# Kernel optimization log

Hardware: AMD Instinct MI355X
Metric: run time of the kernel (lower is better)

The kernel has to match this reference:

```python
import jax, jax.numpy as jnp
import numpy as np

N = 512
B = 128
T = 1000
INP = 6
OUT = 1
DT, TAU = 1.0, 10.0
ALPHA = DT / TAU
SIGMA_REC, SIGMA_INP = 0.05, 0.01
SPECTRAL_RAD = 1.2


def setup_inputs() -> dict:
    key = jax.random.key(0)
    k_u, k_rn, k_in, k_wr, k_wi, k_wo = jax.random.split(key, 6)
    u = jax.random.normal(k_u, (B, T, INP), dtype=jnp.float32)
    # noise pre-scaled as in the torch module: sqrt(2/alpha * sigma^2) * randn
    rec_noise = jnp.sqrt(2.0 / ALPHA * SIGMA_REC ** 2) * jax.random.normal(k_rn, (B, T, N), dtype=jnp.float32)
    inp_noise = jnp.sqrt(2.0 / ALPHA * SIGMA_INP ** 2) * jax.random.normal(k_in, (B, T, INP), dtype=jnp.float32)
    # scaled init connectivity (stand-in for get_connectivity): spectral radius ~ SPECTRAL_RAD
    W_rec = (SPECTRAL_RAD / np.sqrt(N)) * jax.random.normal(k_wr, (N, N), dtype=jnp.float32)
    W_inp = (1.0 / np.sqrt(INP)) * jax.random.normal(k_wi, (N, INP), dtype=jnp.float32)
    W_out = (1.0 / np.sqrt(N)) * jax.random.normal(k_wo, (OUT, N), dtype=jnp.float32)
    y_init = jnp.zeros((N,), dtype=jnp.float32)
    return {"u": u, "rec_noise": rec_noise, "inp_noise": inp_noise,
            "W_rec": W_rec, "W_inp": W_inp, "W_out": W_out, "y_init": y_init}


def _run_dynamics(u, rec_noise, inp_noise, W_rec, W_inp, W_out, y_init):
    alpha = jnp.float32(ALPHA)
    s0 = jnp.broadcast_to(y_init, (u.shape[0], N))  # (B, N)

    def step(s, xs):
        u_t, in_t, rn_t = xs  # (B,INP),(B,INP),(B,N)
        pre = s @ W_rec.T + (u_t + in_t) @ W_inp.T
        s_new = (1.0 - alpha) * s + alpha * (jax.nn.relu(pre) + rn_t)
        return s_new, s_new

    # torch loop runs for i in range(T-1); step i uses inputs/noise at time i
    xs = (jnp.swapaxes(u[:, :-1], 0, 1),
          jnp.swapaxes(inp_noise[:, :-1], 0, 1),
          jnp.swapaxes(rec_noise[:, :-1], 0, 1))
    _, states_tail = jax.lax.scan(step, s0, xs)  # (T-1, B, N)
    states = jnp.concatenate([s0[:, None, :], jnp.swapaxes(states_tail, 0, 1)], axis=1)  # (B, T, N)
    outputs = states @ W_out.T  # (B, T, OUT)
    return states, outputs


def reference(u, rec_noise, inp_noise, W_rec, W_inp, W_out, y_init):
    return _run_dynamics(u, rec_noise, inp_noise, W_rec, W_inp, W_out, y_init)
```

## Files before the change

kernel.cpp:

```cpp
#include <hip/hip_runtime.h>


#define NN 512
#define BB 128
#define TT 1000
#define NIN 6
#define PP 4
#define GG 2
#define NGRP (BB / GG)
#define NWG (PP * NGRP)
#define SLICE (NN / PP)
#define XWORDS (2 * NGRP * GG * NN)
#define WS_NEED (XWORDS * sizeof(unsigned long long))

typedef unsigned long long u64;

__global__ void init_xbuf(u64* xbuf) {
  const int i = blockIdx.x * 256 + threadIdx.x;
  if (i < XWORDS / 2) {
    xbuf[i] = 0xFFFFFFFF00000000ULL;
    xbuf[i + XWORDS / 2] = 0xFFFFFFFF00000000ULL;
  }
}

__device__ __forceinline__ float wave_sum(float v) {
  #pragma unroll
  for (int off = 32; off > 0; off >>= 1) v += __shfl_xor(v, off, 64);
  return v;
}

__device__ __forceinline__ void pin4(float4& a, float4& b, float4& c, float4& d) {
  asm volatile("" : "+v"(a.x), "+v"(a.y), "+v"(a.z), "+v"(a.w),
                    "+v"(b.x), "+v"(b.y), "+v"(b.z), "+v"(b.w),
                    "+v"(c.x), "+v"(c.y), "+v"(c.z), "+v"(c.w),
                    "+v"(d.x), "+v"(d.y), "+v"(d.z), "+v"(d.w));
}

__device__ __forceinline__ u64 xld(const u64* p) {
  return __hip_atomic_load(p, __ATOMIC_RELAXED, __HIP_MEMORY_SCOPE_SYSTEM);
}
__device__ __forceinline__ void xst(u64* p, u64 v) {
  __hip_atomic_store(p, v, __ATOMIC_RELAXED, __HIP_MEMORY_SCOPE_SYSTEM);
}

__global__ __launch_bounds__(512, 1)
void rnn_tagx2(const float* __restrict__ u, const float* __restrict__ rnz,
               const float* __restrict__ inz, const float* __restrict__ Wrec,
               const float* __restrict__ Winp, const float* __restrict__ yinit,
               float* __restrict__ states, u64* __restrict__ xbuf) {
  const int tid = threadIdx.x;
  const int xcd = blockIdx.x & 7;
  const int rest = blockIdx.x >> 3;
  const int p = rest & 3;
  const int g = (rest >> 2) * 8 + xcd;

  const int nq = tid & 31;
  const int n0 = nq << 2;
  const int ks = tid >> 5;
  const int k0 = ks << 5;
  const int ub = (tid >> 7) & 1;
  const int un = tid & 127;
  const int ung = p * SLICE + un;
  const int f1r = tid >> 8, f1b = (tid >> 7) & 1, f1n = tid & 127;
  const int f1q = (p + 1 + f1r) & 3;
  const int f2b = (tid >> 7) & 1, f2n = tid & 127;
  const int f2q = (p + 3) & 3;

  __shared__ __align__(16) float pred[16][GG][SLICE];
  __shared__ __align__(16) float s_all[GG][NN];
  __shared__ float winp_s[SLICE][NIN];
  __shared__ float ubuf[2][GG][NIN];

  float4 w[4][8];
  #pragma unroll
  for (int i = 0; i < 4; ++i) {
    const float* wr = Wrec + (size_t)(p * SLICE + n0 + i) * NN + k0;
    #pragma unroll
    for (int q = 0; q < 8; ++q)
      w[i][q] = *reinterpret_cast<const float4*>(wr + 4 * q);
  }
  for (int i = tid; i < SLICE * NIN; i += 512) {
    const int r = i / NIN, j = i - r * NIN;
    winp_s[r][j] = Winp[(p * SLICE + r) * NIN + j];
  }
  for (int i = tid; i < GG * NN; i += 512)
    s_all[i >> 9][i & 511] = yinit[i & 511];
  for (int i = tid; i < GG * NN; i += 512)
    states[(size_t)(g * GG + (i >> 9)) * TT * NN + (i & 511)] = yinit[i & 511];
  float scur = (tid < 256) ? yinit[ung] : 0.f;
  __syncthreads();

  for (int t = 0; t < TT - 1; ++t) {
    const int par = t & 1;

    #pragma unroll
    for (int i = 0; i < 4; ++i) {
      pin4(w[i][0], w[i][1], w[i][2], w[i][3]);
      pin4(w[i][4], w[i][5], w[i][6], w[i][7]);
    }

    float rnv = 0.f;
    if (tid < 256)
      rnv = rnz[((size_t)(g * GG + ub) * TT + t) * NN + ung];
    if (tid < GG * NIN) {
      const int b = tid / NIN, j = tid - b * NIN;
      const size_t idx = ((size_t)(g * GG + b) * TT + t) * NIN + j;
      ubuf[par][b][j] = u[idx] + inz[idx];
    }

    if (t > 0) {
      const u64* xb = xbuf + ((size_t)par * NGRP + g) * GG * NN;
      const u64* p1 = xb + (size_t)f1b * NN + f1q * SLICE + f1n;
      u64 v1 = xld(p1);
      u64 v2 = 0;
      const u64* p2 = xb + (size_t)f2b * NN + f2q * SLICE + f2n;
      if (tid < 256) v2 = xld(p2);
      while ((int)(v1 >> 32) < t) { __builtin_amdgcn_s_sleep(1); v1 = xld(p1); }
      s_all[f1b][f1q * SLICE + f1n] = __uint_as_float((unsigned)v1);
      if (tid < 256) {
        while ((int)(v2 >> 32) < t) { __builtin_amdgcn_s_sleep(1); v2 = xld(p2); }
        s_all[f2b][f2q * SLICE + f2n] = __uint_as_float((unsigned)v2);
      }
    }
    __syncthreads();

    float a0[GG], a1[GG], a2[GG], a3[GG];
    #pragma unroll
    for (int b = 0; b < GG; ++b) { a0[b] = 0.f; a1[b] = 0.f; a2[b] = 0.f; a3[b] = 0.f; }
    #pragma unroll
    for (int b = 0; b < GG; ++b) {
      #pragma unroll
      for (int q = 0; q < 8; ++q) {
        const float4 sv = *reinterpret_cast<const float4*>(&s_all[b][k0 + 4 * q]);
        a0[b] = fmaf(w[0][q].x, sv.x, a0[b]); a0[b] = fmaf(w[0][q].y, sv.y, a0[b]);
        a0[b] = fmaf(w[0][q].z, sv.z, a0[b]); a0[b] = fmaf(w[0][q].w, sv.w, a0[b]);
        a1[b] = fmaf(w[1][q].x, sv.x, a1[b]); a1[b] = fmaf(w[1][q].y, sv.y, a1[b]);
        a1[b] = fmaf(w[1][q].z, sv.z, a1[b]); a1[b] = fmaf(w[1][q].w, sv.w, a1[b]);
        a2[b] = fmaf(w[2][q].x, sv.x, a2[b]); a2[b] = fmaf(w[2][q].y, sv.y, a2[b]);
        a2[b] = fmaf(w[2][q].z, sv.z, a2[b]); a2[b] = fmaf(w[2][q].w, sv.w, a2[b]);
        a3[b] = fmaf(w[3][q].x, sv.x, a3[b]); a3[b] = fmaf(w[3][q].y, sv.y, a3[b]);
        a3[b] = fmaf(w[3][q].z, sv.z, a3[b]); a3[b] = fmaf(w[3][q].w, sv.w, a3[b]);
      }
    }
    #pragma unroll
    for (int b = 0; b < GG; ++b)
      *reinterpret_cast<float4*>(&pred[ks][b][n0]) =
          make_float4(a0[b], a1[b], a2[b], a3[b]);
    __syncthreads();

    if (tid < 256) {
      float pre = 0.f;
      #pragma unroll
      for (int q = 0; q < 16; ++q) pre += pred[q][ub][un];
      #pragma unroll
      for (int j = 0; j < NIN; ++j)
        pre = fmaf(ubuf[par][ub][j], winp_s[un][j], pre);
      const float sn = 0.9f * scur + 0.1f * (fmaxf(pre, 0.f) + rnv);
      states[((size_t)(g * GG + ub) * TT + t + 1) * NN + ung] = sn;
      const u64 pw = ((u64)(unsigned)(t + 1) << 32) | __float_as_uint(sn);
      xst(&xbuf[(((size_t)((t + 1) & 1) * NGRP + g) * GG + ub) * NN + ung], pw);
      asm volatile("" ::: "memory");
      s_all[ub][ung] = sn;
      scur = sn;
    }
  }
}

__global__ __launch_bounds__(256)
void out_proj(const float* __restrict__ states, const float* __restrict__ Wout,
              float* __restrict__ outputs) {
  const int lane = threadIdx.x & 63;
  const size_t row = (size_t)blockIdx.x * 4 + (threadIdx.x >> 6);
  if (row >= (size_t)BB * TT) return;
  const float* sr = states + row * NN;
  float acc = 0.f;
  #pragma unroll
  for (int h = 0; h < 2; ++h) {
    const float4 sv = *reinterpret_cast<const float4*>(sr + h * 256 + lane * 4);
    const float4 wv = *reinterpret_cast<const float4*>(Wout + h * 256 + lane * 4);
    acc = fmaf(sv.x, wv.x, acc);
    acc = fmaf(sv.y, wv.y, acc);
    acc = fmaf(sv.z, wv.z, acc);
    acc = fmaf(sv.w, wv.w, acc);
  }
  acc = wave_sum(acc);
  if (lane == 0) outputs[row] = acc;
}

__global__ __launch_bounds__(512)
void rnn_fused(const float* __restrict__ u, const float* __restrict__ rnz,
               const float* __restrict__ inz, const float* __restrict__ Wsrc,
               const float* __restrict__ Winp, const float* __restrict__ Wout,
               const float* __restrict__ yinit,
               float* __restrict__ states, float* __restrict__ outputs) {
  const int tid = threadIdx.x;
  const int n4 = tid & 127;
  const int kc = tid >> 7;
  const int b0 = blockIdx.x * 2;
  const int b1 = b0 + 1;

  __shared__ __align__(16) float s[2][NN];
  __shared__ __align__(16) float red[2][128][20];
  __shared__ float ubf[2 * NIN];
  __shared__ float outred[2][8];

  float wi[NIN];
  #pragma unroll
  for (int j = 0; j < NIN; ++j) wi[j] = Winp[tid * NIN + j];
  const float wo = Wout[tid];
  const float yv = yinit[tid];

  s[0][tid] = yv;
  s[1][tid] = yv;
  states[(size_t)(b0 * TT) * NN + tid] = yv;
  states[(size_t)(b1 * TT) * NN + tid] = yv;
  {
    float pzz = wave_sum(yv * wo);
    if ((tid & 63) == 0) outred[0][tid >> 6] = pzz;
  }
  __syncthreads();
  if (tid < 2) {
    float a = 0.f;
    #pragma unroll
    for (int wq = 0; wq < 8; ++wq) a += outred[0][wq];
    outputs[(tid ? b1 : b0) * TT] = a;
  }
  __syncthreads();

  for (int t = 0; t < TT - 1; ++t) {
    const float rn0 = rnz[(size_t)(b0 * TT + t) * NN + tid];
    const float rn1 = rnz[(size_t)(b1 * TT + t) * NN + tid];
    float uv = 0.f;
    if (tid < 2 * NIN) {
      const int b = (tid < NIN) ? b0 : b1;
      const int j = (tid < NIN) ? tid : tid - NIN;
      const int idx = (b * TT + t) * NIN + j;
      uv = u[idx] + inz[idx];
    }
    float a0[4] = {0.f, 0.f, 0.f, 0.f};
    float a1[4] = {0.f, 0.f, 0.f, 0.f};
    const int kbase0 = kc * 128;
    #pragma unroll 4
    for (int j4 = 0; j4 < 32; ++j4) {
      const int kb = kbase0 + j4 * 4;
      const float4 s0v = *reinterpret_cast<const float4*>(&s[0][kb]);
      const float4 s1v = *reinterpret_cast<const float4*>(&s[1][kb]);
      const float s0a[4] = {s0v.x, s0v.y, s0v.z, s0v.w};
      const float s1a[4] = {s1v.x, s1v.y, s1v.z, s1v.w};
      #pragma unroll
      for (int jj = 0; jj < 4; ++jj) {
        const int k = kb + jj;
        const float* pw = Wsrc + (size_t)(n4 << 2) * NN + k;
        float4 wv;
        wv.x = pw[0]; wv.y = pw[NN]; wv.z = pw[2 * NN]; wv.w = pw[3 * NN];
        a0[0] = fmaf(wv.x, s0a[jj], a0[0]);
        a0[1] = fmaf(wv.y, s0a[jj], a0[1]);
        a0[2] = fmaf(wv.z, s0a[jj], a0[2]);
        a0[3] = fmaf(wv.w, s0a[jj], a0[3]);
        a1[0] = fmaf(wv.x, s1a[jj], a1[0]);
        a1[1] = fmaf(wv.y, s1a[jj], a1[1]);
        a1[2] = fmaf(wv.z, s1a[jj], a1[2]);
        a1[3] = fmaf(wv.w, s1a[jj], a1[3]);
      }
    }
    if (tid < 2 * NIN) ubf[tid] = uv;
    *reinterpret_cast<float4*>(&red[0][n4][kc << 2]) =
        make_float4(a0[0], a0[1], a0[2], a0[3]);
    *reinterpret_cast<float4*>(&red[1][n4][kc << 2]) =
        make_float4(a1[0], a1[1], a1[2], a1[3]);
    __syncthreads();
    const int n = tid;
    const int r = n >> 2, c = n & 3;
    float pre0 = (red[0][r][c] + red[0][r][4 + c]) +
                 (red[0][r][8 + c] + red[0][r][12 + c]);
    float pre1 = (red[1][r][c] + red[1][r][4 + c]) +
                 (red[1][r][8 + c] + red[1][r][12 + c]);
    #pragma unroll
    for (int j = 0; j < NIN; ++j) {
      pre0 = fmaf(ubf[j], wi[j], pre0);
      pre1 = fmaf(ubf[NIN + j], wi[j], pre1);
    }
    const float sn0 = 0.9f * s[0][n] + 0.1f * (fmaxf(pre0, 0.f) + rn0);
    const float sn1 = 0.9f * s[1][n] + 0.1f * (fmaxf(pre1, 0.f) + rn1);
    states[(size_t)(b0 * TT + t + 1) * NN + n] = sn0;
    states[(size_t)(b1 * TT + t + 1) * NN + n] = sn1;
    s[0][n] = sn0;
    s[1][n] = sn1;
    float p0 = wave_sum(sn0 * wo);
    float p1 = wave_sum(sn1 * wo);
    if ((tid & 63) == 0) {
      outred[0][tid >> 6] = p0;
      outred[1][tid >> 6] = p1;
    }
    __syncthreads();
    if (tid < 2) {
      float a = 0.f;
      #pragma unroll
      for (int wq = 0; wq < 8; ++wq) a += outred[tid][wq];
      outputs[(tid ? b1 : b0) * TT + t + 1] = a;
    }
  }
}

extern "C" void kernel_launch(void* const* d_in, const int* in_sizes, int n_in,
                              void* d_out, int out_size, void* d_ws, size_t ws_size,
                              hipStream_t stream) {
  const float* u    = (const float*)d_in[0];
  const float* rnz  = (const float*)d_in[1];
  const float* inz  = (const float*)d_in[2];
  const float* Wrec = (const float*)d_in[3];
  const float* Winp = (const float*)d_in[4];
  const float* Wout = (const float*)d_in[5];
  const float* yin  = (const float*)d_in[6];
  float* states  = (float*)d_out;
  float* outputs = states + (size_t)BB * TT * NN;

  if (ws_size >= WS_NEED) {
    u64* xbuf = (u64*)d_ws;
    init_xbuf<<<(XWORDS / 2 + 255) / 256, 256, 0, stream>>>(xbuf);
    rnn_tagx2<<<NWG, 512, 0, stream>>>(u, rnz, inz, Wrec, Winp, yin,
                                       states, xbuf);
    out_proj<<<(BB * TT + 3) / 4, 256, 0, stream>>>(states, Wout, outputs);
  } else {
    rnn_fused<<<BB / 2, 512, 0, stream>>>(u, rnz, inz, Wrec, Winp, Wout,
                                          yin, states, outputs);
  }
}
```

Baseline: 2.862 ms.

## Add fast sc0-scoped exchange buffer with fallback to system-scope polling

Adds a second exchange buffer written and read with inline-asm global loads and stores using the sc0 cache bit instead of system-scope atomics, for cross-workgroup state handoff each timestep. Readers poll the fast buffer a few times and permanently fall back to the system-scope buffer if the tag has not arrived. The aim is to cut the latency of inter-workgroup synchronisation on the serial recurrence. In exchange every state value is written twice, the workspace requirement doubles, and the fast path depends on cache coherence behaviour that may not hold across XCDs.

```diff
diff --git a/kernel.cpp b/kernel.cpp
--- a/kernel.cpp
+++ b/kernel.cpp
@@ -11,16 +11,14 @@
 #define NWG (PP * NGRP)
 #define SLICE (NN / PP)
 #define XWORDS (2 * NGRP * GG * NN)
-#define WS_NEED (XWORDS * sizeof(unsigned long long))
+#define WS_FAST (2 * XWORDS * sizeof(unsigned long long))
+#define WS_SLOW (XWORDS * sizeof(unsigned long long))
 
 typedef unsigned long long u64;
 
-__global__ void init_xbuf(u64* xbuf) {
+__global__ void init_xbuf(u64* xbuf, int nwords) {
   const int i = blockIdx.x * 256 + threadIdx.x;
-  if (i < XWORDS / 2) {
-    xbuf[i] = 0xFFFFFFFF00000000ULL;
-    xbuf[i + XWORDS / 2] = 0xFFFFFFFF00000000ULL;
-  }
+  if (i < nwords) xbuf[i] = 0xFFFFFFFF00000000ULL;
 }
 
 __device__ __forceinline__ float wave_sum(float v) {
@@ -42,12 +40,45 @@
 __device__ __forceinline__ void xst(u64* p, u64 v) {
   __hip_atomic_store(p, v, __ATOMIC_RELAXED, __HIP_MEMORY_SCOPE_SYSTEM);
 }
-
+__device__ __forceinline__ u64 fld(const u64* p) {
+  u64 v;
+  asm volatile("global_load_dwordx2 %0, %1, off sc0\n\ts_waitcnt vmcnt(0)"
+               : "=v"(v) : "v"(p) : "memory");
+  return v;
+}
+__device__ __forceinline__ void fst(u64* p, u64 v) {
+  asm volatile("global_store_dwordx2 %0, %1, off sc0" :: "v"(p), "v"(v)
+               : "memory");
+}
+
+__device__ __forceinline__ u64 pollw(const u64* pf, const u64* ps, int t,
+                                     int& fastok) {
+  u64 v;
+  if (fastok) {
+    v = fld(pf);
+    #pragma unroll 1
+    for (int tr = 0; tr < 4 && (int)(v >> 32) < t; ++tr) {
+      __builtin_amdgcn_s_sleep(1);
+      v = fld(pf);
+    }
+    if ((int)(v >> 32) >= t) return v;
+    fastok = 0;
+  }
+  v = xld(ps);
+  while ((int)(v >> 32) < t) {
+    __builtin_amdgcn_s_sleep(2);
+    v = xld(ps);
+  }
+  return v;
+}
+
+template <bool TWOSIDED>
 __global__ __launch_bounds__(512, 1)
-void rnn_tagx2(const float* __restrict__ u, const float* __restrict__ rnz,
+void rnn_tagx3(const float* __restrict__ u, const float* __restrict__ rnz,
                const float* __restrict__ inz, const float* __restrict__ Wrec,
                const float* __restrict__ Winp, const float* __restrict__ yinit,
-               float* __restrict__ states, u64* __restrict__ xbuf) {
+               float* __restrict__ states, u64* __restrict__ xslow,
+               u64* __restrict__ xfast) {
   const int tid = threadIdx.x;
   const int xcd = blockIdx.x & 7;
   const int rest = blockIdx.x >> 3;
@@ -88,6 +119,7 @@
   for (int i = tid; i < GG * NN; i += 512)
     states[(size_t)(g * GG + (i >> 9)) * TT * NN + (i & 511)] = yinit[i & 511];
   float scur = (tid < 256) ? yinit[ung] : 0.f;
+  int fastok = TWOSIDED ? 1 : 0;
   __syncthreads();
 
   for (int t = 0; t < TT - 1; ++t) {
@@ -109,16 +141,13 @@
     }
 
     if (t > 0) {
-      const u64* xb = xbuf + ((size_t)par * NGRP + g) * GG * NN;
-      const u64* p1 = xb + (size_t)f1b * NN + f1q * SLICE + f1n;
-      u64 v1 = xld(p1);
-      u64 v2 = 0;
-      const u64* p2 = xb + (size_t)f2b * NN + f2q * SLICE + f2n;
-      if (tid < 256) v2 = xld(p2);
-      while ((int)(v1 >> 32) < t) { __builtin_amdgcn_s_sleep(1); v1 = xld(p1); }
+      const size_t base = ((size_t)par * NGRP + g) * GG * NN;
+      const size_t o1 = base + (size_t)f1b * NN + f1q * SLICE + f1n;
+      const u64 v1 = pollw(xfast + o1, xslow + o1, t, fastok);
       s_all[f1b][f1q * SLICE + f1n] = __uint_as_float((unsigned)v1);
       if (tid < 256) {
-        while ((int)(v2 >> 32) < t) { __builtin_amdgcn_s_sleep(1); v2 = xld(p2); }
+        const size_t o2 = base + (size_t)f2b * NN + f2q * SLICE + f2n;
+        const u64 v2 = pollw(xfast + o2, xslow + o2, t, fastok);
         s_all[f2b][f2q * SLICE + f2n] = __uint_as_float((unsigned)v2);
       }
     }
@@ -139,7 +168,7 @@
         a2[b] = fmaf(w[2][q].x, sv.x, a2[b]); a2[b] = fmaf(w[2][q].y, sv.y, a2[b]);
         a2[b] = fmaf(w[2][q].z, sv.z, a2[b]); a2[b] = fmaf(w[2][q].w, sv.w, a2[b]);
         a3[b] = fmaf(w[3][q].x, sv.x, a3[b]); a3[b] = fmaf(w[3][q].y, sv.y, a3[b]);
-        a3[b] = fmaf(w[3][q].z, sv.z, a3[b]); a3[b] = fmaf(w[3][q].w, sv.w, a3[b]);
+        a3[b] = fmaf(w[3][q].w, sv.w, a3[b]); a3[b] = fmaf(w[3][q].z, sv.z, a3[b]);
       }
     }
     #pragma unroll
@@ -158,7 +187,9 @@
       const float sn = 0.9f * scur + 0.1f * (fmaxf(pre, 0.f) + rnv);
       states[((size_t)(g * GG + ub) * TT + t + 1) * NN + ung] = sn;
       const u64 pw = ((u64)(unsigned)(t + 1) << 32) | __float_as_uint(sn);
-      xst(&xbuf[(((size_t)((t + 1) & 1) * NGRP + g) * GG + ub) * NN + ung], pw);
+      const size_t wo = (((size_t)((t + 1) & 1) * NGRP + g) * GG + ub) * NN + ung;
+      if (TWOSIDED) fst(xfast + wo, pw);
+      xst(xslow + wo, pw);
       asm volatile("" ::: "memory");
       s_all[ub][ung] = sn;
       scur = sn;
@@ -315,11 +346,18 @@
   float* states  = (float*)d_out;
   float* outputs = states + (size_t)BB * TT * NN;
 
-  if (ws_size >= WS_NEED) {
-    u64* xbuf = (u64*)d_ws;
-    init_xbuf<<<(XWORDS / 2 + 255) / 256, 256, 0, stream>>>(xbuf);
-    rnn_tagx2<<<NWG, 512, 0, stream>>>(u, rnz, inz, Wrec, Winp, yin,
-                                       states, xbuf);
+  if (ws_size >= WS_FAST) {
+    u64* xslow = (u64*)d_ws;
+    u64* xfast = xslow + XWORDS;
+    init_xbuf<<<(2 * XWORDS + 255) / 256, 256, 0, stream>>>(xslow, 2 * XWORDS);
+    rnn_tagx3<true><<<NWG, 512, 0, stream>>>(u, rnz, inz, Wrec, Winp, yin,
+                                             states, xslow, xfast);
+    out_proj<<<(BB * TT + 3) / 4, 256, 0, stream>>>(states, Wout, outputs);
+  } else if (ws_size >= WS_SLOW) {
+    u64* xslow = (u64*)d_ws;
+    init_xbuf<<<(XWORDS + 255) / 256, 256, 0, stream>>>(xslow, XWORDS);
+    rnn_tagx3<false><<<NWG, 512, 0, stream>>>(u, rnz, inz, Wrec, Winp, yin,
+                                              states, xslow, xslow);
     out_proj<<<(BB * TT + 3) / 4, 256, 0, stream>>>(states, Wout, outputs);
   } else {
     rnn_fused<<<BB / 2, 512, 0, stream>>>(u, rnz, inz, Wrec, Winp, Wout,
```

After: 3.098 ms. 1.08x slower.
